# Performance work log

Measured on AMD Instinct MI355X. Metric: run time of the kernel, lower is better.

The kernel has to match this reference:

```python
import jax, jax.numpy as jnp
import numpy as np

EPS = 1e-30
TEMP = 0.01
DROP_PROB = 0.2


def _gumbel_sigmoid_mask(p, u):
    # drop_prob_mask = sigmoid((log(p+eps)-log(1-p+eps)+log(u+eps)-log(1-u+eps))/temp)
    logit = (jnp.log(p + EPS) - jnp.log(1.0 - p + EPS)
             + jnp.log(u + EPS) - jnp.log(1.0 - u + EPS))
    return 1.0 - jax.nn.sigmoid(logit / TEMP)


def setup_inputs() -> dict:
    key = jax.random.key(0)
    k1, k2, k3, k4, k5 = jax.random.split(key, 5)
    B, H, W, Cin, F, KH, KW = 8, 512, 512, 32, 32, 3, 3
    inputs = jax.random.normal(k1, (B, H, W, Cin), dtype=jnp.float32)
    kernel = jax.random.normal(k2, (KH, KW, Cin, F), dtype=jnp.float32) * 0.05
    bias = jax.random.normal(k3, (F,), dtype=jnp.float32) * 0.05
    unif_c = jax.random.uniform(k4, (B, KH, KW, Cin, F), dtype=jnp.float32)
    unif_b = jax.random.uniform(k5, (B, F), dtype=jnp.float32)
    return {"inputs": inputs, "kernel": kernel, "bias": bias,
            "unif_c": unif_c, "unif_b": unif_b}


def reference(inputs, kernel, bias, unif_c, unif_b):
    B = inputs.shape[0]
    # mask_p = sigmoid(0 + log(0.2/0.8)) = 0.2 (constant)
    p_c = jax.nn.sigmoid(jnp.log(jnp.float32(0.2 / 0.8)))
    mask_c = _gumbel_sigmoid_mask(p_c, unif_c)                 # [B,kh,kw,Cin,F]
    mask_b = _gumbel_sigmoid_mask(jnp.float32(DROP_PROB), unif_b)  # [B,F]
    masked_k = kernel[None] * mask_c                           # [B,kh,kw,Cin,F]
    masked_b = bias[None] * mask_b                             # [B,F]

    def single_conv(x, k):
        # x: [H,W,Cin], k: [kh,kw,Cin,F] -> [H,W,F] ('same' padding, stride 1)
        return jax.lax.conv_general_dilated(
            x[None], k, window_strides=(1, 1), padding='SAME',
            dimension_numbers=('NHWC', 'HWIO', 'NHWC'))[0]

    outputs = jax.vmap(single_conv)(inputs, masked_k)          # [B,H,W,F]
    outputs = outputs + masked_b[:, None, None, :]
    return outputs
```

## Files before the change

### kernel.cpp

```cpp
#include <hip/hip_runtime.h>


typedef unsigned short u16;
typedef unsigned int   u32;
typedef __attribute__((ext_vector_type(4))) unsigned short u16x4;
typedef __attribute__((ext_vector_type(8))) __bf16 bf16x8;
typedef __attribute__((ext_vector_type(4))) float  f32x4;

#define EPSF 1e-30f

__device__ __forceinline__ u16 f2bf(float f) {
    u32 x = __float_as_uint(f);
    x += 0x7fffu + ((x >> 16) & 1u);
    return (u16)(x >> 16);
}
__device__ __forceinline__ float bf2f(u16 h) {
    return __uint_as_float(((u32)h) << 16);
}

__global__ __launch_bounds__(256) void prep_kernel(
    const float* __restrict__ kern, const float* __restrict__ bias,
    const float* __restrict__ unif_c, const float* __restrict__ unif_b,
    u16* __restrict__ kw_hi, u16* __restrict__ kw_lo,
    float* __restrict__ mbias)
{
    int flat = blockIdx.x * 256 + threadIdx.x;
    if (flat < 73728) {
        int f  = flat & 31;
        int ci = (flat >> 5) & 31;
        int t  = (flat >> 10) % 9;
        int b  = flat / 9216;
        float k = kern[flat % 9216];
        float u = unif_c[flat];
        float lp = logf(0.25f);
        float p  = 1.0f / (1.0f + expf(-lp));
        float logit = logf(p + EPSF) - logf(1.0f - p + EPSF)
                    + logf(u + EPSF) - logf(1.0f - u + EPSF);
        float s  = 1.0f / (1.0f + expf(-(logit / 0.01f)));
        float w  = k * (1.0f - s);
        u16 hi = f2bf(w);
        u16 lo = f2bf(w - bf2f(hi));
        int g = ci >> 3, j = ci & 7;
        int dst = (((b * 9 + t) * 4 + g) * 32 + f) * 8 + j;
        kw_hi[dst] = hi;
        kw_lo[dst] = lo;
    } else if (flat < 73728 + 256) {
        int idx = flat - 73728;
        int f = idx & 31;
        float u = unif_b[idx];
        float logit = logf(0.2f + EPSF) - logf(0.8f + EPSF)
                    + logf(u + EPSF) - logf(1.0f - u + EPSF);
        float s = 1.0f / (1.0f + expf(-(logit / 0.01f)));
        mbias[idx] = bias[f] * (1.0f - s);
    }
}

__global__ __launch_bounds__(512) void conv_kernel(
    const float* __restrict__ in,
    const u16* __restrict__ kw_hi, const u16* __restrict__ kw_lo,
    const float* __restrict__ mbias,
    float* __restrict__ out)
{
    __shared__ __align__(16) u16 sAhi[4 * 18 * 18 * 8];
    __shared__ __align__(16) u16 sAlo[4 * 18 * 18 * 8];

    const int b    = blockIdx.z;
    const int ty0  = blockIdx.y * 16;
    const int tx0  = blockIdx.x * 16;
    const int tid  = threadIdx.x;
    const int lane = tid & 63;
    const int wave = tid >> 6;
    const int rgrp = wave & 3;
    const int nh   = wave >> 2;
    const int lm   = lane & 15;
    const int g    = lane >> 4;

    bf16x8 bh[9], bl[9];
    {
        const u16* ph = kw_hi + (b * 9) * 1024;
        const u16* pl = kw_lo + (b * 9) * 1024;
        const int off = (g * 32 + lm + 16 * nh) * 8;
        #pragma unroll
        for (int t = 0; t < 9; ++t) {
            bh[t] = *reinterpret_cast<const bf16x8*>(ph + t * 1024 + off);
            bl[t] = *reinterpret_cast<const bf16x8*>(pl + t * 1024 + off);
        }
    }

    for (int i = tid; i < 2592; i += 512) {
        int p   = i >> 3;
        int row = p / 18;
        int col = p - row * 18;
        int c4  = (i & 7) * 4;
        int gy  = ty0 - 1 + row;
        int gx  = tx0 - 1 + col;
        float4 v = make_float4(0.f, 0.f, 0.f, 0.f);
        if ((unsigned)gy < 512u && (unsigned)gx < 512u) {
            v = *reinterpret_cast<const float4*>(
                in + (((size_t)b * 512 + gy) * 512 + gx) * 32 + c4);
        }
        u16x4 h, l;
        h.x = f2bf(v.x); l.x = f2bf(v.x - bf2f(h.x));
        h.y = f2bf(v.y); l.y = f2bf(v.y - bf2f(h.y));
        h.z = f2bf(v.z); l.z = f2bf(v.z - bf2f(h.z));
        h.w = f2bf(v.w); l.w = f2bf(v.w - bf2f(h.w));
        int gg = c4 >> 3, j0 = c4 & 7;
        int dst = ((gg * 18 + row) * 18 + col) * 8 + j0;
        *reinterpret_cast<u16x4*>(&sAhi[dst]) = h;
        *reinterpret_cast<u16x4*>(&sAlo[dst]) = l;
    }
    __syncthreads();

    f32x4 acc[4];
    #pragma unroll
    for (int r = 0; r < 4; ++r) acc[r] = (f32x4){0.f, 0.f, 0.f, 0.f};

    #pragma unroll
    for (int t = 0; t < 9; ++t) {
        const int ky = t / 3;
        const int kx = t - ky * 3;
        #pragma unroll
        for (int r = 0; r < 4; ++r) {
            const int row = rgrp * 4 + r + ky;
            const int col = lm + kx;
            const int off = ((g * 18 + row) * 18 + col) * 8;
            bf16x8 ah = *reinterpret_cast<const bf16x8*>(&sAhi[off]);
            bf16x8 al = *reinterpret_cast<const bf16x8*>(&sAlo[off]);
            acc[r] = __builtin_amdgcn_mfma_f32_16x16x32_bf16(ah, bh[t], acc[r], 0, 0, 0);
            acc[r] = __builtin_amdgcn_mfma_f32_16x16x32_bf16(al, bh[t], acc[r], 0, 0, 0);
            acc[r] = __builtin_amdgcn_mfma_f32_16x16x32_bf16(ah, bl[t], acc[r], 0, 0, 0);
        }
    }

    const float bsv = mbias[b * 32 + lm + 16 * nh];
    #pragma unroll
    for (int r = 0; r < 4; ++r) {
        const int y = ty0 + rgrp * 4 + r;
        #pragma unroll
        for (int q = 0; q < 4; ++q) {
            const int x = tx0 + g * 4 + q;
            out[(((size_t)b * 512 + y) * 512 + x) * 32 + lm + 16 * nh] =
                acc[r][q] + bsv;
        }
    }
}

extern "C" void kernel_launch(void* const* d_in, const int* in_sizes, int n_in,
                              void* d_out, int out_size, void* d_ws, size_t ws_size,
                              hipStream_t stream) {
    const float* inputs = (const float*)d_in[0];
    const float* kern   = (const float*)d_in[1];
    const float* bias   = (const float*)d_in[2];
    const float* unif_c = (const float*)d_in[3];
    const float* unif_b = (const float*)d_in[4];
    float* out = (float*)d_out;

    u16*   kw_hi = (u16*)d_ws;
    u16*   kw_lo = kw_hi + 73728;
    float* mbias = (float*)(kw_lo + 73728);

    hipLaunchKernelGGL(prep_kernel, dim3(289), dim3(256), 0, stream,
                       kern, bias, unif_c, unif_b, kw_hi, kw_lo, mbias);
    hipLaunchKernelGGL(conv_kernel, dim3(32, 32, 8), dim3(512), 0, stream,
                       inputs, kw_hi, kw_lo, mbias, out);
}
```

Before: 543.6 us.

## Enlarge conv tile to 24 rows and have each wave compute both filter halves

The spatial tile grows from 16 to 24 output rows, which lowers the share of halo rows loaded per output and the number of blocks. Each of the 8 waves now handles 3 rows across all 32 filters instead of 4 rows across 16 filters, so every A fragment read from LDS feeds two MFMA filter halves. Weights are loaded from global memory inside the tap loop rather than kept in registers for the whole kernel. The last row of tiles runs past the image (22*24 > 512) and relies on zero padding plus a guarded store, which wastes some compute, and the per-tap global weight loads can add latency.

```diff
diff --git a/kernel.cpp b/kernel.cpp
--- a/kernel.cpp
+++ b/kernel.cpp
@@ -55,39 +55,30 @@
     }
 }
 
+#define TROWS 24
+#define HROWS 26
+#define ASZ (4 * HROWS * 18 * 8)
+
 __global__ __launch_bounds__(512) void conv_kernel(
     const float* __restrict__ in,
     const u16* __restrict__ kw_hi, const u16* __restrict__ kw_lo,
     const float* __restrict__ mbias,
     float* __restrict__ out)
 {
-    __shared__ __align__(16) u16 sAhi[4 * 18 * 18 * 8];
-    __shared__ __align__(16) u16 sAlo[4 * 18 * 18 * 8];
+    __shared__ __align__(16) u16 sAhi[ASZ];
+    __shared__ __align__(16) u16 sAlo[ASZ];
 
     const int b    = blockIdx.z;
-    const int ty0  = blockIdx.y * 16;
+    const int ty0  = blockIdx.y * TROWS;
     const int tx0  = blockIdx.x * 16;
     const int tid  = threadIdx.x;
     const int lane = tid & 63;
     const int wave = tid >> 6;
-    const int rgrp = wave & 3;
-    const int nh   = wave >> 2;
+    const int wrow = wave * 3;
     const int lm   = lane & 15;
     const int g    = lane >> 4;
 
-    bf16x8 bh[9], bl[9];
-    {
-        const u16* ph = kw_hi + (b * 9) * 1024;
-        const u16* pl = kw_lo + (b * 9) * 1024;
-        const int off = (g * 32 + lm + 16 * nh) * 8;
-        #pragma unroll
-        for (int t = 0; t < 9; ++t) {
-            bh[t] = *reinterpret_cast<const bf16x8*>(ph + t * 1024 + off);
-            bl[t] = *reinterpret_cast<const bf16x8*>(pl + t * 1024 + off);
-        }
-    }
-
-    for (int i = tid; i < 2592; i += 512) {
+    for (int i = tid; i < HROWS * 18 * 8; i += 512) {
         int p   = i >> 3;
         int row = p / 18;
         int col = p - row * 18;
@@ -105,42 +96,61 @@
         h.z = f2bf(v.z); l.z = f2bf(v.z - bf2f(h.z));
         h.w = f2bf(v.w); l.w = f2bf(v.w - bf2f(h.w));
         int gg = c4 >> 3, j0 = c4 & 7;
-        int dst = ((gg * 18 + row) * 18 + col) * 8 + j0;
+        int dst = ((gg * HROWS + row) * 18 + col) * 8 + j0;
         *reinterpret_cast<u16x4*>(&sAhi[dst]) = h;
         *reinterpret_cast<u16x4*>(&sAlo[dst]) = l;
     }
     __syncthreads();
 
-    f32x4 acc[4];
+    f32x4 acc[3][2];
     #pragma unroll
-    for (int r = 0; r < 4; ++r) acc[r] = (f32x4){0.f, 0.f, 0.f, 0.f};
+    for (int r = 0; r < 3; ++r) {
+        acc[r][0] = (f32x4){0.f, 0.f, 0.f, 0.f};
+        acc[r][1] = (f32x4){0.f, 0.f, 0.f, 0.f};
+    }
+
+    const u16* ph = kw_hi + b * 9216;
+    const u16* pl = kw_lo + b * 9216;
+    const int foff0 = (g * 32 + lm) * 8;
+    const int foff1 = foff0 + 128;
 
     #pragma unroll
     for (int t = 0; t < 9; ++t) {
+        const bf16x8 tbh0 = *reinterpret_cast<const bf16x8*>(ph + t * 1024 + foff0);
+        const bf16x8 tbh1 = *reinterpret_cast<const bf16x8*>(ph + t * 1024 + foff1);
+        const bf16x8 tbl0 = *reinterpret_cast<const bf16x8*>(pl + t * 1024 + foff0);
+        const bf16x8 tbl1 = *reinterpret_cast<const bf16x8*>(pl + t * 1024 + foff1);
         const int ky = t / 3;
         const int kx = t - ky * 3;
         #pragma unroll
-        for (int r = 0; r < 4; ++r) {
-            const int row = rgrp * 4 + r + ky;
+        for (int r = 0; r < 3; ++r) {
+            const int row = wrow + r + ky;
             const int col = lm + kx;
-            const int off = ((g * 18 + row) * 18 + col) * 8;
+            const int off = ((g * HROWS + row) * 18 + col) * 8;
             bf16x8 ah = *reinterpret_cast<const bf16x8*>(&sAhi[off]);
             bf16x8 al = *reinterpret_cast<const bf16x8*>(&sAlo[off]);
-            acc[r] = __builtin_amdgcn_mfma_f32_16x16x32_bf16(ah, bh[t], acc[r], 0, 0, 0);
-            acc[r] = __builtin_amdgcn_mfma_f32_16x16x32_bf16(al, bh[t], acc[r], 0, 0, 0);
-            acc[r] = __builtin_amdgcn_mfma_f32_16x16x32_bf16(ah, bl[t], acc[r], 0, 0, 0);
+            acc[r][0] = __builtin_amdgcn_mfma_f32_16x16x32_bf16(ah, tbh0, acc[r][0], 0, 0, 0);
+            acc[r][1] = __builtin_amdgcn_mfma_f32_16x16x32_bf16(ah, tbh1, acc[r][1], 0, 0, 0);
+            acc[r][0] = __builtin_amdgcn_mfma_f32_16x16x32_bf16(al, tbh0, acc[r][0], 0, 0, 0);
+            acc[r][1] = __builtin_amdgcn_mfma_f32_16x16x32_bf16(al, tbh1, acc[r][1], 0, 0, 0);
+            acc[r][0] = __builtin_amdgcn_mfma_f32_16x16x32_bf16(ah, tbl0, acc[r][0], 0, 0, 0);
+            acc[r][1] = __builtin_amdgcn_mfma_f32_16x16x32_bf16(ah, tbl1, acc[r][1], 0, 0, 0);
         }
     }
 
-    const float bsv = mbias[b * 32 + lm + 16 * nh];
+    const float bsv0 = mbias[b * 32 + lm];
+    const float bsv1 = mbias[b * 32 + lm + 16];
     #pragma unroll
-    for (int r = 0; r < 4; ++r) {
-        const int y = ty0 + rgrp * 4 + r;
-        #pragma unroll
-        for (int q = 0; q < 4; ++q) {
-            const int x = tx0 + g * 4 + q;
-            out[(((size_t)b * 512 + y) * 512 + x) * 32 + lm + 16 * nh] =
-                acc[r][q] + bsv;
+    for (int r = 0; r < 3; ++r) {
+        const int y = ty0 + wrow + r;
+        if (y < 512) {
+            #pragma unroll
+            for (int q = 0; q < 4; ++q) {
+                const int x = tx0 + g * 4 + q;
+                const size_t base = (((size_t)b * 512 + y) * 512 + x) * 32;
+                out[base + lm]      = acc[r][0][q] + bsv0;
+                out[base + lm + 16] = acc[r][1][q] + bsv1;
+            }
         }
     }
 }
@@ -161,6 +171,6 @@
 
     hipLaunchKernelGGL(prep_kernel, dim3(289), dim3(256), 0, stream,
                        kern, bias, unif_c, unif_b, kw_hi, kw_lo, mbias);
-    hipLaunchKernelGGL(conv_kernel, dim3(32, 32, 8), dim3(512), 0, stream,
+    hipLaunchKernelGGL(conv_kernel, dim3(32, 22, 8), dim3(512), 0, stream,
                        inputs, kw_hi, kw_lo, mbias, out);
 }
```

After: 498.4 us. -8.3%, faster.
